# Performance work log

Measured on AMD Instinct MI355X. Metric: run time of the kernel, lower is better.

The kernel has to match this reference:

```python
import jax, jax.numpy as jnp
import numpy as np

BN_EPS = 1e-5


def maxpool2(x):
    # 2x2 max pool, stride 2: (B,C,H,W) -> (B,C,H//2,W//2)
    B, C, H, W = x.shape
    return x.reshape(B, C, H // 2, 2, W // 2, 2).max(axis=(3, 5))


def setup_inputs() -> dict:
    key = jax.random.key(0)
    ks = jax.random.split(key, 6)
    B, C, H, W = 4, 64, 96, 96   # in_dim = 64
    K, OD = 64, 64               # key_dim, out_dim
    sc = lambda fan: 1.0 / np.sqrt(fan)
    return {
        "c2": jax.random.normal(ks[0], (B, C, H, W), jnp.float32),
        "x": jax.random.normal(ks[1], (B, C, H, W), jnp.float32),
        # edge_att: Conv2d(2C->OD, 1x1, no bias) -> BN -> ReLU -> Conv2d(OD->1, 1x1) -> Sigmoid
        "w_ea1": jax.random.normal(ks[2], (OD, 2 * C), jnp.float32) * sc(2 * C),
        "bn_w": jnp.ones((OD,), jnp.float32),
        "bn_b": jnp.zeros((OD,), jnp.float32),
        "bn_m": jnp.zeros((OD,), jnp.float32),
        "bn_v": jnp.ones((OD,), jnp.float32),
        "w_ea2": jax.random.normal(ks[3], (1, OD), jnp.float32) * sc(OD),
        "b_ea2": jnp.zeros((1,), jnp.float32),
        # query_conv (shared for query AND key in the original forward)
        "w_q": jax.random.normal(ks[4], (K, C), jnp.float32) * sc(C),
        "b_q": jnp.zeros((K,), jnp.float32),
        "gamma": jnp.full((1,), 0.5, jnp.float32),
    }


def reference(c2, x, w_ea1, bn_w, bn_b, bn_m, bn_v, w_ea2, b_ea2, w_q, b_q, gamma):
    xp = maxpool2(x)        # (B,C,Hp,Wp)
    c2p = maxpool2(c2)
    B, C, H, W = x.shape
    Hp, Wp = xp.shape[2], xp.shape[3]

    # edge attention gate on pooled features -> (B,1,Hp,Wp)
    cat = jnp.concatenate([c2p, xp], axis=1)                       # (B,2C,Hp,Wp)
    h = jnp.einsum('oc,bchw->bohw', w_ea1, cat)
    bn_scale = (bn_w / jnp.sqrt(bn_v + BN_EPS))[None, :, None, None]
    h = jax.nn.relu((h - bn_m[None, :, None, None]) * bn_scale + bn_b[None, :, None, None])
    ea = jax.nn.sigmoid(jnp.einsum('oc,bchw->bohw', w_ea2, h) + b_ea2[None, :, None, None])

    # query at full res, key at pooled res (SAME conv weights, as in the source)
    q = jnp.einsum('kc,bchw->bkhw', w_q, x) + b_q[None, :, None, None]    # (B,K,H,W)
    k = jnp.einsum('kc,bchw->bkhw', w_q, xp) + b_q[None, :, None, None]   # (B,K,Hp,Wp)

    pq = q.reshape(B, -1, H * W)        # (B,K,N)
    pk = k.reshape(B, -1, Hp * Wp)      # (B,K,M)
    energy = jnp.einsum('bkn,bkm->bnm', pq, pk)                    # (B,N,M)
    attn = jax.nn.softmax(energy * ea.reshape(B, 1, Hp * Wp), axis=-1)

    v = xp.reshape(B, C, Hp * Wp)                                   # (B,C,M)
    out = jnp.einsum('bcm,bnm->bcn', v, attn).reshape(B, C, H, W)
    return gamma[0] * out + x
```

## Files before the change

### kernel.cpp

```cpp
#include <hip/hip_runtime.h>
#include <stdint.h>

#define B_ 4
#define C_ 64
#define H_ 96
#define W_ 96
#define HP_ 48
#define WP_ 48
#define N_ (H_*W_)
#define M_ (HP_*WP_)
#define KD_ 64
#define OD_ 64
#define BN_EPS 1e-5f
#define LOG2E 1.4426950408889634f
#define SHIFT2 28.853900817779268f
#define QT_ 48
#define QB_ (N_/QT_)

typedef __bf16 bf16_t;
typedef bf16_t bf16x8 __attribute__((ext_vector_type(8)));
typedef bf16_t bf16x4 __attribute__((ext_vector_type(4)));
typedef float f32x4 __attribute__((ext_vector_type(4)));
typedef short short4v __attribute__((ext_vector_type(4)));

static __device__ __forceinline__ unsigned short f2bf(float f) {
    unsigned int u = __builtin_bit_cast(unsigned int, f);
    u += 0x7fffu + ((u >> 16) & 1u);
    return (unsigned short)(u >> 16);
}

static __device__ __forceinline__ f32x4 mfma16_bf16(short4v a, short4v b, f32x4 c) {
#if __has_builtin(__builtin_amdgcn_mfma_f32_16x16x16bf16_1k)
    return __builtin_amdgcn_mfma_f32_16x16x16bf16_1k(a, b, c, 0, 0, 0);
#else
    return c;
#endif
}

__global__ __launch_bounds__(256) void prep_kernel(
    const float* __restrict__ x, const float* __restrict__ c2,
    const float* __restrict__ wq, const float* __restrict__ bq,
    const float* __restrict__ w1, const float* __restrict__ bnw, const float* __restrict__ bnb,
    const float* __restrict__ bnm, const float* __restrict__ bnv,
    const float* __restrict__ w2, const float* __restrict__ b2,
    unsigned short* __restrict__ kb, unsigned short* __restrict__ vb, float* __restrict__ ea) {

    __shared__ float lw1[OD_*2*C_];
    __shared__ float lwq[KD_*C_];
    __shared__ float xs[C_*33];
    __shared__ float c2s[C_*33];
    __shared__ float red[8][32];

    int tid = threadIdx.x;
    int b = blockIdx.x / 72;
    int m0 = (blockIdx.x % 72) * 32;

    for (int i = tid; i < OD_*2*C_; i += 256) lw1[i] = w1[i];
    for (int i = tid; i < KD_*C_; i += 256) lwq[i] = wq[i];
    for (int j = tid; j < 2048; j += 256) {
        int c = j >> 5, p = j & 31;
        int m = m0 + p;
        int hp = m / WP_, wp = m % WP_;
        size_t base = ((size_t)(b*C_ + c)*H_ + 2*hp)*W_ + 2*wp;
        const float* px = x + base;
        float mx = fmaxf(fmaxf(px[0], px[1]), fmaxf(px[W_], px[W_+1]));
        xs[c*33 + p] = mx;
        vb[(size_t)(b*C_ + c)*M_ + m] = f2bf(mx);
        const float* pc = c2 + base;
        c2s[c*33 + p] = fmaxf(fmaxf(pc[0], pc[1]), fmaxf(pc[W_], pc[W_+1]));
    }
    __syncthreads();

    int ml = tid & 31, oz = tid >> 5;
    int m = m0 + ml;

    float h[8] = {0,0,0,0,0,0,0,0};
    for (int c = 0; c < C_; c += 4) {
        float x0 = xs[c*33+ml], x1 = xs[(c+1)*33+ml], x2 = xs[(c+2)*33+ml], x3 = xs[(c+3)*33+ml];
        #pragma unroll
        for (int oi = 0; oi < 8; oi++) {
            const float4 wv = *(const float4*)&lwq[(oz*8 + oi)*C_ + c];
            h[oi] = fmaf(wv.x, x0, fmaf(wv.y, x1, fmaf(wv.z, x2, fmaf(wv.w, x3, h[oi]))));
        }
    }
    unsigned short tmp[8];
    #pragma unroll
    for (int oi = 0; oi < 8; oi++) tmp[oi] = f2bf(h[oi] + bq[oz*8 + oi]);
    *(uint4*)&kb[((size_t)b*M_ + m)*KD_ + oz*8] = *(const uint4*)tmp;

    float g[8] = {0,0,0,0,0,0,0,0};
    for (int c = 0; c < 2*C_; c += 4) {
        const float* srcb = (c < C_) ? &c2s[c*33] : &xs[(c - C_)*33];
        float x0 = srcb[ml], x1 = srcb[33+ml], x2 = srcb[66+ml], x3 = srcb[99+ml];
        #pragma unroll
        for (int oi = 0; oi < 8; oi++) {
            const float4 wv = *(const float4*)&lw1[(oz*8 + oi)*(2*C_) + c];
            g[oi] = fmaf(wv.x, x0, fmaf(wv.y, x1, fmaf(wv.z, x2, fmaf(wv.w, x3, g[oi]))));
        }
    }
    float z = 0.f;
    #pragma unroll
    for (int oi = 0; oi < 8; oi++) {
        int o = oz*8 + oi;
        float sc = bnw[o] * rsqrtf(bnv[o] + BN_EPS);
        float t = (g[oi] - bnm[o]) * sc + bnb[o];
        z += w2[o] * fmaxf(t, 0.f);
    }
    red[oz][ml] = z;
    __syncthreads();
    if (oz == 0) {
        float s = b2[0];
        #pragma unroll
        for (int i = 0; i < 8; i++) s += red[i][ml];
        ea[(size_t)b*M_ + m] = LOG2E / (1.f + __builtin_amdgcn_exp2f(-s * LOG2E));
    }
}

__global__ __launch_bounds__(256) void qk_kernel(const float* __restrict__ in, const float* __restrict__ wq,
    const float* __restrict__ bq, unsigned short* __restrict__ outb) {
    __shared__ float lw[KD_*C_];
    for (int i = threadIdx.x; i < KD_*C_; i += 256) lw[i] = wq[i];
    __syncthreads();
    int ml = threadIdx.x & 31, oz = threadIdx.x >> 5;
    int pg = blockIdx.x * 32 + ml;
    float h[8] = {0,0,0,0,0,0,0,0};
    const float* src = in + ((size_t)(pg / N_))*C_*N_ + (pg % N_);
    for (int c = 0; c < C_; c += 4) {
        float x0 = src[(size_t)c*N_], x1 = src[(size_t)(c+1)*N_];
        float x2 = src[(size_t)(c+2)*N_], x3 = src[(size_t)(c+3)*N_];
        #pragma unroll
        for (int oi = 0; oi < 8; oi++) {
            const float4 wv = *(const float4*)&lw[(oz*8 + oi)*C_ + c];
            h[oi] = fmaf(wv.x, x0, fmaf(wv.y, x1, fmaf(wv.z, x2, fmaf(wv.w, x3, h[oi]))));
        }
    }
    unsigned short tmp[8];
    #pragma unroll
    for (int oi = 0; oi < 8; oi++) tmp[oi] = f2bf(h[oi] + bq[oz*8 + oi]);
    *(uint4*)&outb[(size_t)pg*KD_ + oz*8] = *(const uint4*)tmp;
}

__global__ __launch_bounds__(256, 3) void attn_kernel(
    const unsigned short* __restrict__ qb, const unsigned short* __restrict__ kb,
    const unsigned short* __restrict__ vb, const float* __restrict__ ea,
    const float* __restrict__ x, const float* __restrict__ gamma_p, float* __restrict__ out) {

    __shared__ __align__(16) char smem[36864];

    int tid = threadIdx.x;
    int wave = tid >> 6, lane = tid & 63, quad = lane >> 4, l16 = lane & 15;
    int blk = blockIdx.x;
    int b = (blk & 7) >> 1;
    int n_base = ((blk & 1) * (QB_/2) + (blk >> 3)) * QT_;

    bf16x8 qf[3][2];
    #pragma unroll
    for (int qi = 0; qi < 3; qi++) {
        const unsigned short* qp = qb + ((size_t)b*N_ + n_base + qi*16 + l16)*KD_;
        qf[qi][0] = __builtin_bit_cast(bf16x8, *(const uint4*)(qp + quad*8));
        qf[qi][1] = __builtin_bit_cast(bf16x8, *(const uint4*)(qp + 32 + quad*8));
    }

    f32x4 o2[3][4];
    #pragma unroll
    for (int qi = 0; qi < 3; qi++)
        #pragma unroll
        for (int ct = 0; ct < 4; ct++) o2[qi][ct] = (f32x4){0.f,0.f,0.f,0.f};
    float ls[3] = {0.f,0.f,0.f};

    const unsigned short* kbB = kb + (size_t)b*M_*KD_;
    const unsigned short* vbB = vb + (size_t)b*C_*M_;
    const float* eaB = ea + (size_t)b*M_;

    int r0 = tid >> 3, g8 = (tid & 7) << 3;
    uint4 kA, kB, vA, vB;

    {
        kA = *(const uint4*)(kbB + (size_t)r0*KD_ + g8);
        kB = *(const uint4*)(kbB + (size_t)(r0+32)*KD_ + g8);
        vA = *(const uint4*)(vbB + (size_t)r0*M_ + g8);
        vB = *(const uint4*)(vbB + (size_t)(r0+32)*M_ + g8);
        unsigned short* k0 = (unsigned short*)smem;
        unsigned short* v0 = (unsigned short*)(smem + 9216);
        *(uint4*)(k0 + r0*72 + g8) = kA;
        *(uint4*)(k0 + (r0+32)*72 + g8) = kB;
        *(uint4*)(v0 + r0*72 + g8) = vA;
        *(uint4*)(v0 + (r0+32)*72 + g8) = vB;
    }
    __syncthreads();

    for (int mt = 0; mt < M_/64; mt++) {
        int cur = mt & 1;
        if (mt < M_/64 - 1) {
            int mb = (mt+1) * 64;
            kA = *(const uint4*)(kbB + (size_t)(mb + r0)*KD_ + g8);
            kB = *(const uint4*)(kbB + (size_t)(mb + r0 + 32)*KD_ + g8);
            vA = *(const uint4*)(vbB + (size_t)r0*M_ + mb + g8);
            vB = *(const uint4*)(vbB + (size_t)(r0+32)*M_ + mb + g8);
        }
        unsigned short* kc = (unsigned short*)(smem + cur*18432);
        unsigned short* vc = (unsigned short*)(smem + cur*18432 + 9216);

        f32x4 e4 = *(const f32x4*)(eaB + mt*64 + wave*16 + quad*4);

        bf16x8 kf0 = __builtin_bit_cast(bf16x8, *(const uint4*)(kc + (wave*16 + l16)*72 + quad*8));
        bf16x8 kf1 = __builtin_bit_cast(bf16x8, *(const uint4*)(kc + (wave*16 + l16)*72 + 32 + quad*8));
        short4v va[4];
        #pragma unroll
        for (int ct = 0; ct < 4; ct++)
            va[ct] = *(const short4v*)(vc + (ct*16 + l16)*72 + wave*16 + quad*4);

        f32x4 st[3];
        #pragma unroll
        for (int qi = 0; qi < 3; qi++) {
            f32x4 z = (f32x4){0.f,0.f,0.f,0.f};
            z = __builtin_amdgcn_mfma_f32_16x16x32_bf16(kf0, qf[qi][0], z, 0, 0, 0);
            z = __builtin_amdgcn_mfma_f32_16x16x32_bf16(kf1, qf[qi][1], z, 0, 0, 0);
            st[qi] = z;
        }

        short4v pk[3];
        #pragma unroll
        for (int qi = 0; qi < 3; qi++) {
            f32x4 p;
            p[0] = __builtin_amdgcn_exp2f(fmaf(st[qi][0], e4[0], -SHIFT2));
            p[1] = __builtin_amdgcn_exp2f(fmaf(st[qi][1], e4[1], -SHIFT2));
            p[2] = __builtin_amdgcn_exp2f(fmaf(st[qi][2], e4[2], -SHIFT2));
            p[3] = __builtin_amdgcn_exp2f(fmaf(st[qi][3], e4[3], -SHIFT2));
            ls[qi] += (p[0] + p[1]) + (p[2] + p[3]);
            pk[qi] = __builtin_bit_cast(short4v, __builtin_convertvector(p, bf16x4));
        }

        #pragma unroll
        for (int ct = 0; ct < 4; ct++)
            #pragma unroll
            for (int qi = 0; qi < 3; qi++)
                o2[qi][ct] = mfma16_bf16(va[ct], pk[qi], o2[qi][ct]);

        if (mt < M_/64 - 1) {
            int nxt = 1 - cur;
            unsigned short* kd = (unsigned short*)(smem + nxt*18432);
            unsigned short* vd = (unsigned short*)(smem + nxt*18432 + 9216);
            *(uint4*)(kd + r0*72 + g8) = kA;
            *(uint4*)(kd + (r0+32)*72 + g8) = kB;
            *(uint4*)(vd + r0*72 + g8) = vA;
            *(uint4*)(vd + (r0+32)*72 + g8) = vB;
        }
        __syncthreads();
    }

    float* o_red0 = (float*)smem;
    float* o_red1 = o_red0 + 48*68;
    float* l_red  = o_red1 + 48*68;

    #pragma unroll
    for (int qi = 0; qi < 3; qi++) {
        ls[qi] += __shfl_xor(ls[qi], 16);
        ls[qi] += __shfl_xor(ls[qi], 32);
    }
    if (lane < 16) {
        #pragma unroll
        for (int qi = 0; qi < 3; qi++) l_red[wave*48 + qi*16 + lane] = ls[qi];
    }
    if (wave < 2) {
        float* od = (wave == 0) ? o_red0 : o_red1;
        #pragma unroll
        for (int qi = 0; qi < 3; qi++)
            #pragma unroll
            for (int ct = 0; ct < 4; ct++)
                *(f32x4*)&od[(qi*16 + l16)*68 + ct*16 + quad*4] = o2[qi][ct];
    }
    __syncthreads();
    if (wave >= 2) {
        float* od = (wave == 2) ? o_red0 : o_red1;
        #pragma unroll
        for (int qi = 0; qi < 3; qi++)
            #pragma unroll
            for (int ct = 0; ct < 4; ct++) {
                f32x4* p = (f32x4*)&od[(qi*16 + l16)*68 + ct*16 + quad*4];
                *p += o2[qi][ct];
            }
    }
    __syncthreads();
    if (tid < 48) {
        float s = (l_red[tid] + l_red[48 + tid]) + (l_red[96 + tid] + l_red[144 + tid]);
        l_red[tid] = 1.f / s;
    }
    __syncthreads();

    float gmm = gamma_p[0];
    int c = tid >> 2, q4 = tid & 3;
    const float* xrow = x + ((size_t)b*C_ + c)*N_ + n_base;
    float* orow = out + ((size_t)b*C_ + c)*N_ + n_base;
    #pragma unroll
    for (int i = 0; i < 3; i++) {
        int q0 = q4*4 + i*16;
        float4 xv = *(const float4*)(xrow + q0);
        float4 ov;
        float v0 = (o_red0[(q0+0)*68 + c] + o_red1[(q0+0)*68 + c]) * l_red[q0+0];
        float v1 = (o_red0[(q0+1)*68 + c] + o_red1[(q0+1)*68 + c]) * l_red[q0+1];
        float v2 = (o_red0[(q0+2)*68 + c] + o_red1[(q0+2)*68 + c]) * l_red[q0+2];
        float v3 = (o_red0[(q0+3)*68 + c] + o_red1[(q0+3)*68 + c]) * l_red[q0+3];
        ov.x = fmaf(gmm, v0, xv.x);
        ov.y = fmaf(gmm, v1, xv.y);
        ov.z = fmaf(gmm, v2, xv.z);
        ov.w = fmaf(gmm, v3, xv.w);
        *(float4*)(orow + q0) = ov;
    }
}

extern "C" void kernel_launch(void* const* d_in, const int* in_sizes, int n_in,
                              void* d_out, int out_size, void* d_ws, size_t ws_size,
                              hipStream_t stream) {
    const float* c2    = (const float*)d_in[0];
    const float* x     = (const float*)d_in[1];
    const float* w_ea1 = (const float*)d_in[2];
    const float* bn_w  = (const float*)d_in[3];
    const float* bn_b  = (const float*)d_in[4];
    const float* bn_m  = (const float*)d_in[5];
    const float* bn_v  = (const float*)d_in[6];
    const float* w_ea2 = (const float*)d_in[7];
    const float* b_ea2 = (const float*)d_in[8];
    const float* w_q   = (const float*)d_in[9];
    const float* b_q   = (const float*)d_in[10];
    const float* gamma = (const float*)d_in[11];
    float* out = (float*)d_out;

    char* ws = (char*)d_ws;
    float* ea            = (float*)(ws + 0);
    unsigned short* qb   = (unsigned short*)(ws + 36864);
    unsigned short* kb   = (unsigned short*)(ws + 4755456);
    unsigned short* vb   = (unsigned short*)(ws + 5935104);

    prep_kernel<<<dim3((B_*M_)/32), dim3(256), 0, stream>>>(x, c2, w_q, b_q,
        w_ea1, bn_w, bn_b, bn_m, bn_v, w_ea2, b_ea2, kb, vb, ea);
    qk_kernel<<<dim3((B_*N_)/32), dim3(256), 0, stream>>>(x, w_q, b_q, qb);
    attn_kernel<<<dim3(B_*QB_), dim3(256), 0, stream>>>(qb, kb, vb, ea, x, gamma, out);
}
```

Baseline: 168.2 us.

## Load K/V fragments directly from global into registers, drop LDS staging and barriers

The attention loop no longer stages K and V tiles through double-buffered shared memory with a __syncthreads per tile. Each wave now loads its own MFMA fragments straight from global memory into registers, one tile ahead. The softmax row sums move from scalar adds plus cross-lane shuffles to an extra MFMA against a vector of ones. This removes LDS traffic and barriers and shrinks shared memory, which may allow more resident blocks. In exchange, global loads become narrower and less coalesced, V is read with strided 8-byte accesses, and each block re-reads K/V through cache.

```diff
diff --git a/kernel.cpp b/kernel.cpp
--- a/kernel.cpp
+++ b/kernel.cpp
@@ -145,7 +145,7 @@
     const unsigned short* __restrict__ vb, const float* __restrict__ ea,
     const float* __restrict__ x, const float* __restrict__ gamma_p, float* __restrict__ out) {
 
-    __shared__ __align__(16) char smem[36864];
+    __shared__ __align__(16) char smem[26880];
 
     int tid = threadIdx.x;
     int wave = tid >> 6, lane = tid & 63, quad = lane >> 4, l16 = lane & 15;
@@ -162,53 +162,45 @@
     }
 
     f32x4 o2[3][4];
-    #pragma unroll
-    for (int qi = 0; qi < 3; qi++)
+    f32x4 lacc[3];
+    #pragma unroll
+    for (int qi = 0; qi < 3; qi++) {
+        lacc[qi] = (f32x4){0.f,0.f,0.f,0.f};
         #pragma unroll
         for (int ct = 0; ct < 4; ct++) o2[qi][ct] = (f32x4){0.f,0.f,0.f,0.f};
-    float ls[3] = {0.f,0.f,0.f};
-
-    const unsigned short* kbB = kb + (size_t)b*M_*KD_;
-    const unsigned short* vbB = vb + (size_t)b*C_*M_;
-    const float* eaB = ea + (size_t)b*M_;
-
-    int r0 = tid >> 3, g8 = (tid & 7) << 3;
-    uint4 kA, kB, vA, vB;
-
-    {
-        kA = *(const uint4*)(kbB + (size_t)r0*KD_ + g8);
-        kB = *(const uint4*)(kbB + (size_t)(r0+32)*KD_ + g8);
-        vA = *(const uint4*)(vbB + (size_t)r0*M_ + g8);
-        vB = *(const uint4*)(vbB + (size_t)(r0+32)*M_ + g8);
-        unsigned short* k0 = (unsigned short*)smem;
-        unsigned short* v0 = (unsigned short*)(smem + 9216);
-        *(uint4*)(k0 + r0*72 + g8) = kA;
-        *(uint4*)(k0 + (r0+32)*72 + g8) = kB;
-        *(uint4*)(v0 + r0*72 + g8) = vA;
-        *(uint4*)(v0 + (r0+32)*72 + g8) = vB;
-    }
-    __syncthreads();
+    }
+    const short one_bf = (short)0x3F80;
+    short4v ones = (short4v){one_bf, one_bf, one_bf, one_bf};
+
+    const unsigned short* kW = kb + ((size_t)b*M_ + wave*16 + l16)*KD_ + quad*8;
+    const unsigned short* vW = vb + (size_t)b*C_*M_ + (size_t)(l16)*M_ + wave*16 + quad*4;
+    const float* eaW = ea + (size_t)b*M_ + wave*16 + quad*4;
+
+    uint4 kf0r = *(const uint4*)(kW);
+    uint4 kf1r = *(const uint4*)(kW + 32);
+    uint2 var[4];
+    #pragma unroll
+    for (int ct = 0; ct < 4; ct++)
+        var[ct] = *(const uint2*)(vW + (size_t)(ct*16)*M_);
+    f32x4 e4r = *(const f32x4*)(eaW);
 
     for (int mt = 0; mt < M_/64; mt++) {
-        int cur = mt & 1;
+        bf16x8 kf0 = __builtin_bit_cast(bf16x8, kf0r);
+        bf16x8 kf1 = __builtin_bit_cast(bf16x8, kf1r);
+        short4v va[4];
+        #pragma unroll
+        for (int ct = 0; ct < 4; ct++) va[ct] = __builtin_bit_cast(short4v, var[ct]);
+        f32x4 e4 = e4r;
+
         if (mt < M_/64 - 1) {
             int mb = (mt+1) * 64;
-            kA = *(const uint4*)(kbB + (size_t)(mb + r0)*KD_ + g8);
-            kB = *(const uint4*)(kbB + (size_t)(mb + r0 + 32)*KD_ + g8);
-            vA = *(const uint4*)(vbB + (size_t)r0*M_ + mb + g8);
-            vB = *(const uint4*)(vbB + (size_t)(r0+32)*M_ + mb + g8);
-        }
-        unsigned short* kc = (unsigned short*)(smem + cur*18432);
-        unsigned short* vc = (unsigned short*)(smem + cur*18432 + 9216);
-
-        f32x4 e4 = *(const f32x4*)(eaB + mt*64 + wave*16 + quad*4);
-
-        bf16x8 kf0 = __builtin_bit_cast(bf16x8, *(const uint4*)(kc + (wave*16 + l16)*72 + quad*8));
-        bf16x8 kf1 = __builtin_bit_cast(bf16x8, *(const uint4*)(kc + (wave*16 + l16)*72 + 32 + quad*8));
-        short4v va[4];
-        #pragma unroll
-        for (int ct = 0; ct < 4; ct++)
-            va[ct] = *(const short4v*)(vc + (ct*16 + l16)*72 + wave*16 + quad*4);
+            kf0r = *(const uint4*)(kW + (size_t)mb*KD_);
+            kf1r = *(const uint4*)(kW + (size_t)mb*KD_ + 32);
+            #pragma unroll
+            for (int ct = 0; ct < 4; ct++)
+                var[ct] = *(const uint2*)(vW + (size_t)(ct*16)*M_ + mb);
+            e4r = *(const f32x4*)(eaW + mb);
+        }
 
         f32x4 st[3];
         #pragma unroll
@@ -227,7 +219,6 @@
             p[1] = __builtin_amdgcn_exp2f(fmaf(st[qi][1], e4[1], -SHIFT2));
             p[2] = __builtin_amdgcn_exp2f(fmaf(st[qi][2], e4[2], -SHIFT2));
             p[3] = __builtin_amdgcn_exp2f(fmaf(st[qi][3], e4[3], -SHIFT2));
-            ls[qi] += (p[0] + p[1]) + (p[2] + p[3]);
             pk[qi] = __builtin_bit_cast(short4v, __builtin_convertvector(p, bf16x4));
         }
 
@@ -236,31 +227,18 @@
             #pragma unroll
             for (int qi = 0; qi < 3; qi++)
                 o2[qi][ct] = mfma16_bf16(va[ct], pk[qi], o2[qi][ct]);
-
-        if (mt < M_/64 - 1) {
-            int nxt = 1 - cur;
-            unsigned short* kd = (unsigned short*)(smem + nxt*18432);
-            unsigned short* vd = (unsigned short*)(smem + nxt*18432 + 9216);
-            *(uint4*)(kd + r0*72 + g8) = kA;
-            *(uint4*)(kd + (r0+32)*72 + g8) = kB;
-            *(uint4*)(vd + r0*72 + g8) = vA;
-            *(uint4*)(vd + (r0+32)*72 + g8) = vB;
-        }
-        __syncthreads();
+        #pragma unroll
+        for (int qi = 0; qi < 3; qi++)
+            lacc[qi] = mfma16_bf16(ones, pk[qi], lacc[qi]);
     }
 
     float* o_red0 = (float*)smem;
     float* o_red1 = o_red0 + 48*68;
     float* l_red  = o_red1 + 48*68;
 
-    #pragma unroll
-    for (int qi = 0; qi < 3; qi++) {
-        ls[qi] += __shfl_xor(ls[qi], 16);
-        ls[qi] += __shfl_xor(ls[qi], 32);
-    }
     if (lane < 16) {
         #pragma unroll
-        for (int qi = 0; qi < 3; qi++) l_red[wave*48 + qi*16 + lane] = ls[qi];
+        for (int qi = 0; qi < 3; qi++) l_red[wave*48 + qi*16 + l16] = lacc[qi][0];
     }
     if (wave < 2) {
         float* od = (wave == 0) ? o_red0 : o_red1;
```

Result: slower. 206.4 us (+22.7%).
